# Kernel optimization log

Hardware: AMD Instinct MI355X
Metric: run time of the kernel (lower is better)

Reference implementation:

```python
import jax, jax.numpy as jnp
import numpy as np
from jax import lax

B, T, V, L = 256, 512, 256, 64
EPS = 1e-7  # keras backend epsilon used by ctc_batch_cost
NEG = -1e30  # log(0) surrogate, safe in float32


def setup_inputs() -> dict:
    key = jax.random.key(0)
    k1, k2 = jax.random.split(key)
    # labels in [0, V-1): class V-1 is reserved for the CTC blank
    y_true = jax.random.randint(k1, (B, L), 0, V - 1)
    # ctc_batch_cost expects probabilities (softmax output)
    logits = jax.random.normal(k2, (B, T, V), dtype=jnp.float32)
    y_pred = jax.nn.softmax(logits, axis=-1)
    return {"y_true": y_true, "y_pred": y_pred}


def reference(y_true, y_pred):
    """Keras ctc_batch_cost: per-example CTC negative log-likelihood, shape [B,1].

    Matches TF semantics: blank = V-1, log(y_pred + eps), full input/label lengths,
    merge-repeated forward DP in log space.
    """
    b, t, v = y_pred.shape
    l = y_true.shape[1]
    S = 2 * l + 1  # extended label: blank-interleaved
    blank = v - 1

    logp = jnp.log(y_pred + EPS)  # [B,T,V]

    # extended label sequence z: blank at even positions, labels at odd
    ext = jnp.full((b, S), blank, dtype=y_true.dtype).at[:, 1::2].set(y_true)  # [B,S]

    # lp[b,t,s] = logp[b,t,ext[b,s]]
    idx = jnp.broadcast_to(ext[:, None, :], (b, t, S))
    lp = jnp.take_along_axis(logp, idx, axis=2)  # [B,T,S]

    # skip transition s-2 -> s allowed iff z[s] != blank and z[s] != z[s-2]
    ext_m2 = jnp.concatenate([jnp.full((b, 2), -1, dtype=ext.dtype), ext[:, :-2]], axis=1)
    skip = (ext != blank) & (ext != ext_m2)  # [B,S]

    # alpha at t=0: only first blank or first label reachable
    alpha0 = jnp.full((b, S), NEG, dtype=logp.dtype)
    alpha0 = alpha0.at[:, 0].set(lp[:, 0, 0]).at[:, 1].set(lp[:, 0, 1])

    neg1 = jnp.full((b, 1), NEG, dtype=logp.dtype)
    neg2 = jnp.full((b, 2), NEG, dtype=logp.dtype)

    def step(alpha, lpt):
        a1 = jnp.concatenate([neg1, alpha[:, :-1]], axis=1)
        a2 = jnp.concatenate([neg2, alpha[:, :-2]], axis=1)
        m = jnp.logaddexp(alpha, a1)
        m = jnp.where(skip, jnp.logaddexp(m, a2), m)
        return m + lpt, None

    lp_t = jnp.moveaxis(lp[:, 1:], 1, 0)  # [T-1, B, S] time-major
    alphaT, _ = lax.scan(step, alpha0, lp_t)

    loss = -jnp.logaddexp(alphaT[:, -1], alphaT[:, -2])  # [B]
    return loss[:, None]
```

## Files before the change

kernel.cpp:

```cpp
#include <hip/hip_runtime.h>
#include <math.h>


#define BB   256
#define TI   512
#define VV   256
#define LL   64
#define CH   32
#define NCH  (TI / CH)
#define EPSF 1e-7f
#define LN2F 0.6931471805599453f

#if __has_builtin(__builtin_amdgcn_logf)
__device__ __forceinline__ float flog2(float x) { return __builtin_amdgcn_logf(x); }
#else
__device__ __forceinline__ float flog2(float x) { return __log2f(x); }
#endif

template <int CTRL>
__device__ __forceinline__ float dppf(float oldv, float v) {
    return __int_as_float(__builtin_amdgcn_update_dpp(
        __float_as_int(oldv), __float_as_int(v), CTRL, 0xF, 0xF, false));
}
__device__ __forceinline__ float shup0(float x) { return dppf<0x138>(0.0f, x); }

struct DP {
    float a0, a1, a128;
    float C;
    float f, fs;
    float skipf;
    int   lane;
};

__device__ __forceinline__ void rescale(DP& d) {
    float m  = fmaxf(fmaxf(d.a0, d.a1), d.a128);
    int   mi    = __float_as_int(m);
    int   ebits = mi & 0x7f800000;
    bool  dead  = (ebits == 0);
    float s = __int_as_float((254 << 23) - ebits);
    s = dead ? 1.0f : s;
    d.a0 *= s; d.a1 *= s; d.a128 *= s;
    float Ei  = (float)((mi >> 23) - 127);
    float Cm1 = shup0(d.C);
    d.C = dead ? Cm1 : (d.C + Ei);
    float Cm1b = shup0(d.C);
    int dCi = (int)(Cm1b - d.C);
    int e = dCi + 127;
    e = e < 0 ? 0 : (e > 254 ? 254 : e);
    float fn = __int_as_float(e << 23);
    d.f  = (d.lane == 0) ? 0.0f : fn;
    d.fs = d.f * d.skipf;
}

__device__ __forceinline__ void dp_step(DP& d, float pb, float pl) {
    float pa1 = shup0(d.a1);
    float s01 = d.a0 + d.a1;
    float na0   = fmaf(pa1, d.f,  d.a0) * pb;
    float na1   = fmaf(pa1, d.fs, s01)  * pl;
    float na128 = (d.a128 + d.a1) * pb;
    d.a0 = na0; d.a1 = na1; d.a128 = na128;
}

template <bool PA, bool FIRST>
__device__ __forceinline__ void dp_chunk(DP& d, const float (&pb)[CH],
                                         const float (&pl)[CH]) {
    #pragma unroll
    for (int tt = 0; tt < CH; ++tt) {
        if (FIRST && tt == 0) {
            d.a0 = (d.lane == 0) ? pb[0] : 0.0f;
            d.a1 = (d.lane == 0) ? pl[0] : 0.0f;
        } else {
            dp_step(d, pb[tt], pl[tt]);
        }
        if (PA || (tt & 7) == 7) rescale(d);
    }
}

__device__ __forceinline__ void load_chunk(const float* pbase, const float* lbase,
                                           int c, float (&pb)[CH], float (&pl)[CH]) {
    const float* pp = pbase + c * CH * VV;
    const float* ll = lbase + c * CH * VV;
    #pragma unroll
    for (int i = 0; i < CH; ++i) {
        pb[i] = pp[i * VV] + EPSF;
        pl[i] = ll[i * VV] + EPSF;
    }
}

__global__ __launch_bounds__(64) void ctc_kernel(
        const int* __restrict__ y_true,
        const float* __restrict__ y_pred,
        float* __restrict__ out) {
    const int b    = blockIdx.x;
    const int lane = threadIdx.x;
    const float* src = y_pred + (size_t)b * TI * VV;

    const int myLab   = y_true[b * LL + lane];
    const int prevLab = __shfl_up(myLab, 1);

    DP d;
    d.lane  = lane;
    d.skipf = (lane == 0 || myLab != prevLab) ? 1.0f : 0.0f;
    d.a0 = 0.0f; d.a1 = 0.0f; d.a128 = 0.0f;
    d.C = 0.0f; d.f = 0.0f; d.fs = 0.0f;

    const float* pbase = src + (VV - 1);
    const float* lbase = src + myLab;

    float b0p[CH], b0l[CH], b1p[CH], b1l[CH];

    load_chunk(pbase, lbase, 0, b0p, b0l);
    load_chunk(pbase, lbase, 1, b1p, b1l);
    dp_chunk<true, true >(d, b0p, b0l);
    load_chunk(pbase, lbase, 2, b0p, b0l);
    dp_chunk<true, false>(d, b1p, b1l);
    load_chunk(pbase, lbase, 3, b1p, b1l);
    dp_chunk<true, false>(d, b0p, b0l);
    load_chunk(pbase, lbase, 4, b0p, b0l);
    dp_chunk<true, false>(d, b1p, b1l);

    for (int c = 4; c < NCH; c += 2) {
        load_chunk(pbase, lbase, c + 1, b1p, b1l);
        dp_chunk<false, false>(d, b0p, b0l);
        if (c + 2 < NCH) load_chunk(pbase, lbase, c + 2, b0p, b0l);
        dp_chunk<false, false>(d, b1p, b1l);
    }

    if (lane == 63) {
        float tail = fmaxf(d.a128 + d.a1, 1e-37f);
        out[b] = -LN2F * (d.C + flog2(tail));
    }
}

extern "C" void kernel_launch(void* const* d_in, const int* in_sizes, int n_in,
                              void* d_out, int out_size, void* d_ws, size_t ws_size,
                              hipStream_t stream) {
    const int*   y_true = (const int*)d_in[0];
    const float* y_pred = (const float*)d_in[1];
    float*       out    = (float*)d_out;
    ctc_kernel<<<dim3(BB), dim3(64), 0, stream>>>(y_true, y_pred, out);
}
```

Measured before the change: 201.2 us.

## Split CTC kernel into producer and consumer waves with LDS ring buffer

The kernel now runs two waves per block. Wave 1 prefetches probability chunks from global memory into a 4-slot shared-memory ring two chunks ahead, and wave 0 reads each chunk from LDS and runs the serial DP recurrence. The aim is to take global-load latency and register-resident double buffers off the DP wave's critical path. In exchange it adds a __syncthreads per chunk, LDS traffic, and double the threads per block.

```diff
diff --git a/kernel.cpp b/kernel.cpp
--- a/kernel.cpp
+++ b/kernel.cpp
@@ -76,57 +76,75 @@
     }
 }
 
-__device__ __forceinline__ void load_chunk(const float* pbase, const float* lbase,
-                                           int c, float (&pb)[CH], float (&pl)[CH]) {
-    const float* pp = pbase + c * CH * VV;
-    const float* ll = lbase + c * CH * VV;
+__device__ __forceinline__ void fill_chunk(const float* __restrict__ src,
+                                           int lab, int cc, int lane,
+                                           float* __restrict__ pbuf,
+                                           float* __restrict__ lbuf) {
+    const float* rowbase = src + (size_t)cc * CH * VV;
+    const int r = lane & 31;
+    float bv = rowbase[r * VV + (VV - 1)];
+    float lv[CH];
     #pragma unroll
-    for (int i = 0; i < CH; ++i) {
-        pb[i] = pp[i * VV] + EPSF;
-        pl[i] = ll[i * VV] + EPSF;
-    }
+    for (int i = 0; i < CH; ++i)
+        lv[i] = rowbase[i * VV + lab];
+    if (lane < 32) pbuf[r] = bv + EPSF;
+    #pragma unroll
+    for (int i = 0; i < CH; ++i)
+        lbuf[i * 64 + lane] = lv[i] + EPSF;
 }
 
-__global__ __launch_bounds__(64) void ctc_kernel(
+__global__ __launch_bounds__(128) void ctc_kernel(
         const int* __restrict__ y_true,
         const float* __restrict__ y_pred,
         float* __restrict__ out) {
+    __shared__ float pbuf[4][CH];
+    __shared__ float lbuf[4][CH * 64];
+
     const int b    = blockIdx.x;
-    const int lane = threadIdx.x;
+    const int tid  = threadIdx.x;
+    const int lane = tid & 63;
+    const int wave = tid >> 6;
     const float* src = y_pred + (size_t)b * TI * VV;
 
-    const int myLab   = y_true[b * LL + lane];
-    const int prevLab = __shfl_up(myLab, 1);
+    const int lab = y_true[b * LL + lane];
 
     DP d;
-    d.lane  = lane;
-    d.skipf = (lane == 0 || myLab != prevLab) ? 1.0f : 0.0f;
+    d.lane = lane;
+    {
+        const int prevLab = __shfl_up(lab, 1);
+        d.skipf = (lane == 0 || lab != prevLab) ? 1.0f : 0.0f;
+    }
     d.a0 = 0.0f; d.a1 = 0.0f; d.a128 = 0.0f;
     d.C = 0.0f; d.f = 0.0f; d.fs = 0.0f;
 
-    const float* pbase = src + (VV - 1);
-    const float* lbase = src + myLab;
+    if (wave == 1) {
+        fill_chunk(src, lab, 0, lane, pbuf[0], lbuf[0]);
+        fill_chunk(src, lab, 1, lane, pbuf[1], lbuf[1]);
+    }
+    __syncthreads();
 
-    float b0p[CH], b0l[CH], b1p[CH], b1l[CH];
-
-    load_chunk(pbase, lbase, 0, b0p, b0l);
-    load_chunk(pbase, lbase, 1, b1p, b1l);
-    dp_chunk<true, true >(d, b0p, b0l);
-    load_chunk(pbase, lbase, 2, b0p, b0l);
-    dp_chunk<true, false>(d, b1p, b1l);
-    load_chunk(pbase, lbase, 3, b1p, b1l);
-    dp_chunk<true, false>(d, b0p, b0l);
-    load_chunk(pbase, lbase, 4, b0p, b0l);
-    dp_chunk<true, false>(d, b1p, b1l);
-
-    for (int c = 4; c < NCH; c += 2) {
-        load_chunk(pbase, lbase, c + 1, b1p, b1l);
-        dp_chunk<false, false>(d, b0p, b0l);
-        if (c + 2 < NCH) load_chunk(pbase, lbase, c + 2, b0p, b0l);
-        dp_chunk<false, false>(d, b1p, b1l);
+    for (int c = 0; c < NCH; ++c) {
+        if (wave == 1) {
+            if (c + 2 < NCH)
+                fill_chunk(src, lab, c + 2, lane,
+                           pbuf[(c + 2) & 3], lbuf[(c + 2) & 3]);
+        } else {
+            float pb[CH], pl[CH];
+            const float* pp = pbuf[c & 3];
+            const float* ll = lbuf[c & 3] + lane;
+            #pragma unroll
+            for (int i = 0; i < CH; ++i) {
+                pb[i] = pp[i];
+                pl[i] = ll[i * 64];
+            }
+            if (c == 0)      dp_chunk<true,  true >(d, pb, pl);
+            else if (c < 4)  dp_chunk<true,  false>(d, pb, pl);
+            else             dp_chunk<false, false>(d, pb, pl);
+        }
+        __syncthreads();
     }
 
-    if (lane == 63) {
+    if (wave == 0 && lane == 63) {
         float tail = fmaxf(d.a128 + d.a1, 1e-37f);
         out[b] = -LN2F * (d.C + flog2(tail));
     }
@@ -138,5 +156,5 @@
     const int*   y_true = (const int*)d_in[0];
     const float* y_pred = (const float*)d_in[1];
     float*       out    = (float*)d_out;
-    ctc_kernel<<<dim3(BB), dim3(64), 0, stream>>>(y_true, y_pred, out);
+    ctc_kernel<<<dim3(BB), dim3(128), 0, stream>>>(y_true, y_pred, out);
 }
```

Result: faster. 196.2 us (-2.5%).
